# Optimization experiments

Hardware: AMD Instinct MI355X
Metric: run time of the kernel (lower is better)

Reference implementation:

```python
import jax, jax.numpy as jnp
import numpy as np

N_NODES = 100000
N_EDGES = 6400000
F_IN, F_HID, F_OUT = 5, 5, 10


def setup_inputs() -> dict:
    key = jax.random.key(0)
    ks = jax.random.split(key, 9)
    x = jax.random.normal(ks[0], (N_NODES, F_IN), dtype=jnp.float32)
    src = jax.random.randint(ks[1], (N_EDGES,), 0, N_NODES, dtype=jnp.int32)
    dst = jax.random.randint(ks[2], (N_EDGES,), 0, N_NODES, dtype=jnp.int32)
    s1 = 1.0 / np.sqrt(F_IN)
    s2 = 1.0 / np.sqrt(F_HID)
    W_self1 = jax.random.uniform(ks[3], (F_IN, F_HID), jnp.float32, -s1, s1)
    W_neigh1 = jax.random.uniform(ks[4], (F_IN, F_HID), jnp.float32, -s1, s1)
    b1 = jnp.zeros((F_HID,), jnp.float32)
    W_self2 = jax.random.uniform(ks[5], (F_HID, F_OUT), jnp.float32, -s2, s2)
    W_neigh2 = jax.random.uniform(ks[6], (F_HID, F_OUT), jnp.float32, -s2, s2)
    b2 = jnp.zeros((F_OUT,), jnp.float32)
    return {"x": x, "src": src, "dst": dst,
            "W_self1": W_self1, "W_neigh1": W_neigh1, "b1": b1,
            "W_self2": W_self2, "W_neigh2": W_neigh2, "b2": b2}


def _sage_mean(h, src, dst, W_self, W_neigh, b):
    # DGL SAGEConv (mean): out = h @ W_self + mean_{u->v}(h_u) @ W_neigh + b
    msg = h[src]                                        # [E, F] gather
    agg = jax.ops.segment_sum(msg, dst, num_segments=N_NODES)   # [N, F]
    deg = jax.ops.segment_sum(jnp.ones((src.shape[0],), h.dtype), dst,
                              num_segments=N_NODES)     # [N]
    h_neigh = agg / jnp.maximum(deg, 1.0)[:, None]
    return h @ W_self + h_neigh @ W_neigh + b


def reference(x, src, dst, W_self1, W_neigh1, b1, W_self2, W_neigh2, b2):
    h = jax.nn.sigmoid(_sage_mean(x, src, dst, W_self1, W_neigh1, b1))
    out = jax.nn.sigmoid(_sage_mean(h, src, dst, W_self2, W_neigh2, b2))
    return out
```

## Files before the change

kernel.cpp:

```cpp
#include <hip/hip_runtime.h>
#include <math.h>


#define F_IN  5
#define F_HID 5
#define F_OUT 10

#define NBSHIFT 7
#define NPB     (1 << NBSHIFT)
#define MAXNB   1024
#define PBLK    1024
#define CHUNK   8192
#define BSTRIDE 8928
#define SBLK    512
#define LPN2    8
#define LBLK    256

__global__ void init_cursors(int* __restrict__ bcursor, int NB) {
    int t = threadIdx.x;
    if (t < NB) bcursor[t] = t * BSTRIDE;
}

__global__ void partition(const int* __restrict__ src, const int* __restrict__ dst,
                          int* __restrict__ bcursor, int* __restrict__ packed,
                          int E, int NB) {
    __shared__ int h[MAXNB], s[MAXNB], excl[MAXNB], adj[MAXNB];
    __shared__ int buf[CHUNK];
    __shared__ unsigned char dlow[CHUNK];
    int t = threadIdx.x;
    h[t] = 0;
    __syncthreads();
    int base = blockIdx.x * CHUNK;
    int end  = min(base + CHUNK, E);
    for (int i = base + t; i < end; i += PBLK)
        atomicAdd(&h[dst[i] >> NBSHIFT], 1);
    __syncthreads();
    s[t] = h[t];
    __syncthreads();
    for (int off = 1; off < PBLK; off <<= 1) {
        int v = (t >= off) ? s[t - off] : 0;
        __syncthreads();
        s[t] += v;
        __syncthreads();
    }
    excl[t] = s[t] - h[t];
    __syncthreads();
    if (t < NB) {
        int cb = h[t];
        int go = cb ? atomicAdd(&bcursor[t], cb) : 0;
        adj[t] = go - excl[t];
    }
    __syncthreads();
    for (int i = base + t; i < end; i += PBLK) {
        int d = dst[i];
        int b = d >> NBSHIFT;
        int p = atomicAdd(&excl[b], 1);
        buf[p]  = src[i] | (b << 17);
        dlow[p] = (unsigned char)(d & (NPB - 1));
    }
    __syncthreads();
    int cnt = end - base;
    for (int p = t; p < cnt; p += PBLK) {
        int e = buf[p];
        int b = e >> 17;
        packed[adj[b] + p] = (e & 0x1FFFF) | ((int)dlow[p] << 17);
    }
}

__device__ __forceinline__ float sigmoidf(float v) {
    return 1.0f / (1.0f + __expf(-v));
}

__global__ void sortagg1(const float* __restrict__ x, int* __restrict__ packed,
                         const int* __restrict__ bcursor,
                         const float* __restrict__ Ws, const float* __restrict__ Wn,
                         const float* __restrict__ bias,
                         float* __restrict__ hp, int* __restrict__ starts,
                         int* __restrict__ degs, int N) {
    __shared__ int buf[BSTRIDE];
    __shared__ int nhist[NPB], ncur[NPB], nst[NPB];
    int b = blockIdx.x, t = threadIdx.x;
    int s0  = b * BSTRIDE;
    int cnt = min(bcursor[b] - s0, BSTRIDE);
    if (t < NPB) nhist[t] = 0;
    __syncthreads();
    for (int i = t; i < cnt; i += SBLK)
        atomicAdd(&nhist[(packed[s0 + i] >> 17) & (NPB - 1)], 1);
    __syncthreads();
    int v = (t < NPB) ? nhist[t] : 0;
    if (t < NPB) ncur[t] = v;
    __syncthreads();
    for (int off = 1; off < NPB; off <<= 1) {
        int u = (t < NPB && t >= off) ? ncur[t - off] : 0;
        __syncthreads();
        if (t < NPB) ncur[t] += u;
        __syncthreads();
    }
    if (t < NPB) {
        int ex = ncur[t] - v;
        nst[t]  = ex;
        ncur[t] = ex;
        int node = (b << NBSHIFT) + t;
        if (node < N) { starts[node] = s0 + ex; degs[node] = v; }
    }
    __syncthreads();
    for (int i = t; i < cnt; i += SBLK) {
        int e = packed[s0 + i];
        int p = atomicAdd(&ncur[(e >> 17) & (NPB - 1)], 1);
        buf[p] = e;
    }
    __syncthreads();
    for (int i = t; i < cnt; i += SBLK)
        packed[s0 + i] = buf[i] & 0x1FFFF;
    int sub = t & 3, ln = t >> 2;
    int node = (b << NBSHIFT) + ln;
    float a0 = 0, a1 = 0, a2 = 0, a3 = 0, a4 = 0;
    int dg = 0;
    if (node < N) {
        int st = nst[ln];
        dg = nhist[ln];
        for (int k = sub; k < dg; k += 4) {
            int u = buf[st + k] & 0x1FFFF;
            const float* fr = x + (size_t)u * 5;
            float4 a = *(const float4*)fr;
            float  e4 = fr[4];
            a0 += a.x; a1 += a.y; a2 += a.z; a3 += a.w; a4 += e4;
        }
    }
    #pragma unroll
    for (int off = 2; off > 0; off >>= 1) {
        a0 += __shfl_down(a0, off, 4);
        a1 += __shfl_down(a1, off, 4);
        a2 += __shfl_down(a2, off, 4);
        a3 += __shfl_down(a3, off, 4);
        a4 += __shfl_down(a4, off, 4);
    }
    if (sub != 0 || node >= N) return;
    float rd = 1.0f / fmaxf((float)dg, 1.0f);
    float ni[F_IN] = { a0 * rd, a1 * rd, a2 * rd, a3 * rd, a4 * rd };
    float xi[F_IN];
    const float* xr = x + (size_t)node * 5;
    #pragma unroll
    for (int f = 0; f < F_IN; ++f) xi[f] = xr[f];
    #pragma unroll
    for (int j = 0; j < F_HID; ++j) {
        float acc = bias[j];
        #pragma unroll
        for (int f = 0; f < F_IN; ++f)
            acc += xi[f] * Ws[f * F_HID + j] + ni[f] * Wn[f * F_HID + j];
        hp[(size_t)node * 8 + j] = sigmoidf(acc);
    }
}

__global__ void layer2(const float* __restrict__ hp, const int* __restrict__ eidx,
                       const int* __restrict__ starts, const int* __restrict__ degs,
                       const float* __restrict__ Ws, const float* __restrict__ Wn,
                       const float* __restrict__ b,
                       float* __restrict__ out, int N) {
    int tid = blockIdx.x * blockDim.x + threadIdx.x;
    int v   = tid >> 3;
    int sub = threadIdx.x & (LPN2 - 1);
    if (v >= N) return;
    int st = starts[v], dg = degs[v];
    float s0 = 0, s1 = 0, s2 = 0, s3 = 0, s4 = 0;
    for (int k = sub; k < dg; k += LPN2) {
        int u = eidx[st + k];
        const float4 a = *(const float4*)(hp + (size_t)u * 8);
        float a4 = hp[(size_t)u * 8 + 4];
        s0 += a.x; s1 += a.y; s2 += a.z; s3 += a.w; s4 += a4;
    }
    #pragma unroll
    for (int off = LPN2 / 2; off > 0; off >>= 1) {
        s0 += __shfl_down(s0, off, LPN2);
        s1 += __shfl_down(s1, off, LPN2);
        s2 += __shfl_down(s2, off, LPN2);
        s3 += __shfl_down(s3, off, LPN2);
        s4 += __shfl_down(s4, off, LPN2);
    }
    if (sub != 0) return;
    float rd = 1.0f / fmaxf((float)dg, 1.0f);
    float ni[F_HID] = { s0 * rd, s1 * rd, s2 * rd, s3 * rd, s4 * rd };
    float hi[F_HID];
    #pragma unroll
    for (int f = 0; f < F_HID; ++f) hi[f] = hp[(size_t)v * 8 + f];
    #pragma unroll
    for (int j = 0; j < F_OUT; ++j) {
        float acc = b[j];
        #pragma unroll
        for (int f = 0; f < F_HID; ++f)
            acc += hi[f] * Ws[f * F_OUT + j] + ni[f] * Wn[f * F_OUT + j];
        out[(size_t)v * F_OUT + j] = sigmoidf(acc);
    }
}

extern "C" void kernel_launch(void* const* d_in, const int* in_sizes, int n_in,
                              void* d_out, int out_size, void* d_ws, size_t ws_size,
                              hipStream_t stream) {
    const float* x   = (const float*)d_in[0];
    const int*   src = (const int*)d_in[1];
    const int*   dst = (const int*)d_in[2];
    const float* Ws1 = (const float*)d_in[3];
    const float* Wn1 = (const float*)d_in[4];
    const float* b1  = (const float*)d_in[5];
    const float* Ws2 = (const float*)d_in[6];
    const float* Wn2 = (const float*)d_in[7];
    const float* b2  = (const float*)d_in[8];
    float* out = (float*)d_out;

    const int N  = in_sizes[0] / F_IN;
    const int E  = in_sizes[1];
    const int NB = (N + NPB - 1) >> NBSHIFT;

    int*   bcursor = (int*)d_ws;
    int*   starts  = bcursor + 1024;
    int*   degs    = starts + N;
    int*   packed  = degs + N;
    float* hp      = (float*)(packed + (size_t)NB * BSTRIDE);

    const int ablocks = (E + CHUNK - 1) / CHUNK;
    const int lgrid   = ((size_t)N * LPN2 + LBLK - 1) / LBLK;

    init_cursors<<<1, 1024, 0, stream>>>(bcursor, NB);
    partition<<<ablocks, PBLK, 0, stream>>>(src, dst, bcursor, packed, E, NB);
    sortagg1<<<NB, SBLK, 0, stream>>>(x, packed, bcursor, Ws1, Wn1, b1,
                                      hp, starts, degs, N);
    layer2<<<lgrid, LBLK, 0, stream>>>(hp, packed, starts, degs, Ws2, Wn2, b2, out, N);
}
```

Measured before the change: 242.3 us.

## Halve bucket size, cache packed edges in registers, compact hidden features

```diff
diff --git a/kernel.cpp b/kernel.cpp
--- a/kernel.cpp
+++ b/kernel.cpp
@@ -6,49 +6,55 @@
 #define F_HID 5
 #define F_OUT 10
 
-#define NBSHIFT 7
+#define NBSHIFT 6
 #define NPB     (1 << NBSHIFT)
-#define MAXNB   1024
+#define MAXNB   1664
 #define PBLK    1024
-#define CHUNK   8192
-#define BSTRIDE 8928
+#define CHUNK   4096
+#define BSTRIDE 4608
 #define SBLK    512
+#define SPT     9
 #define LPN2    8
-#define LBLK    256
+#define LBLK    512
 
 __global__ void init_cursors(int* __restrict__ bcursor, int NB) {
-    int t = threadIdx.x;
+    int t = blockIdx.x * blockDim.x + threadIdx.x;
     if (t < NB) bcursor[t] = t * BSTRIDE;
 }
 
 __global__ void partition(const int* __restrict__ src, const int* __restrict__ dst,
                           int* __restrict__ bcursor, int* __restrict__ packed,
                           int E, int NB) {
-    __shared__ int h[MAXNB], s[MAXNB], excl[MAXNB], adj[MAXNB];
+    __shared__ int h[MAXNB], excl[MAXNB], adj[MAXNB];
+    __shared__ int scanTmp[PBLK];
     __shared__ int buf[CHUNK];
     __shared__ unsigned char dlow[CHUNK];
     int t = threadIdx.x;
-    h[t] = 0;
+    for (int i = t; i < MAXNB; i += PBLK) h[i] = 0;
     __syncthreads();
     int base = blockIdx.x * CHUNK;
     int end  = min(base + CHUNK, E);
     for (int i = base + t; i < end; i += PBLK)
         atomicAdd(&h[dst[i] >> NBSHIFT], 1);
     __syncthreads();
-    s[t] = h[t];
+    int a0 = h[2 * t];
+    int a1 = h[2 * t + 1];
+    scanTmp[t] = a0 + a1;
     __syncthreads();
     for (int off = 1; off < PBLK; off <<= 1) {
-        int v = (t >= off) ? s[t - off] : 0;
-        __syncthreads();
-        s[t] += v;
-        __syncthreads();
-    }
-    excl[t] = s[t] - h[t];
-    __syncthreads();
-    if (t < NB) {
-        int cb = h[t];
-        int go = cb ? atomicAdd(&bcursor[t], cb) : 0;
-        adj[t] = go - excl[t];
+        int v = (t >= off) ? scanTmp[t - off] : 0;
+        __syncthreads();
+        scanTmp[t] += v;
+        __syncthreads();
+    }
+    int pairExcl = (t == 0) ? 0 : scanTmp[t - 1];
+    excl[2 * t]     = pairExcl;
+    excl[2 * t + 1] = pairExcl + a0;
+    __syncthreads();
+    for (int i = t; i < NB; i += PBLK) {
+        int cb = h[i];
+        int go = cb ? atomicAdd(&bcursor[i], cb) : 0;
+        adj[i] = go - excl[i];
     }
     __syncthreads();
     for (int i = base + t; i < end; i += PBLK) {
@@ -84,8 +90,16 @@
     int cnt = min(bcursor[b] - s0, BSTRIDE);
     if (t < NPB) nhist[t] = 0;
     __syncthreads();
-    for (int i = t; i < cnt; i += SBLK)
-        atomicAdd(&nhist[(packed[s0 + i] >> 17) & (NPB - 1)], 1);
+    int myv[SPT];
+    #pragma unroll
+    for (int j = 0; j < SPT; ++j) {
+        int i = t + j * SBLK;
+        if (i < cnt) {
+            int e = packed[s0 + i];
+            myv[j] = e;
+            atomicAdd(&nhist[(e >> 17) & (NPB - 1)], 1);
+        }
+    }
     __syncthreads();
     int v = (t < NPB) ? nhist[t] : 0;
     if (t < NPB) ncur[t] = v;
@@ -104,22 +118,26 @@
         if (node < N) { starts[node] = s0 + ex; degs[node] = v; }
     }
     __syncthreads();
-    for (int i = t; i < cnt; i += SBLK) {
-        int e = packed[s0 + i];
-        int p = atomicAdd(&ncur[(e >> 17) & (NPB - 1)], 1);
-        buf[p] = e;
+    #pragma unroll
+    for (int j = 0; j < SPT; ++j) {
+        int i = t + j * SBLK;
+        if (i < cnt) {
+            int e = myv[j];
+            int p = atomicAdd(&ncur[(e >> 17) & (NPB - 1)], 1);
+            buf[p] = e;
+        }
     }
     __syncthreads();
     for (int i = t; i < cnt; i += SBLK)
         packed[s0 + i] = buf[i] & 0x1FFFF;
-    int sub = t & 3, ln = t >> 2;
+    int sub = t & 7, ln = t >> 3;
     int node = (b << NBSHIFT) + ln;
     float a0 = 0, a1 = 0, a2 = 0, a3 = 0, a4 = 0;
     int dg = 0;
     if (node < N) {
         int st = nst[ln];
         dg = nhist[ln];
-        for (int k = sub; k < dg; k += 4) {
+        for (int k = sub; k < dg; k += 8) {
             int u = buf[st + k] & 0x1FFFF;
             const float* fr = x + (size_t)u * 5;
             float4 a = *(const float4*)fr;
@@ -128,12 +146,12 @@
         }
     }
     #pragma unroll
-    for (int off = 2; off > 0; off >>= 1) {
-        a0 += __shfl_down(a0, off, 4);
-        a1 += __shfl_down(a1, off, 4);
-        a2 += __shfl_down(a2, off, 4);
-        a3 += __shfl_down(a3, off, 4);
-        a4 += __shfl_down(a4, off, 4);
+    for (int off = 4; off > 0; off >>= 1) {
+        a0 += __shfl_down(a0, off, 8);
+        a1 += __shfl_down(a1, off, 8);
+        a2 += __shfl_down(a2, off, 8);
+        a3 += __shfl_down(a3, off, 8);
+        a4 += __shfl_down(a4, off, 8);
     }
     if (sub != 0 || node >= N) return;
     float rd = 1.0f / fmaxf((float)dg, 1.0f);
@@ -148,7 +166,7 @@
         #pragma unroll
         for (int f = 0; f < F_IN; ++f)
             acc += xi[f] * Ws[f * F_HID + j] + ni[f] * Wn[f * F_HID + j];
-        hp[(size_t)node * 8 + j] = sigmoidf(acc);
+        hp[(size_t)node * 5 + j] = sigmoidf(acc);
     }
 }
 
@@ -165,8 +183,9 @@
     float s0 = 0, s1 = 0, s2 = 0, s3 = 0, s4 = 0;
     for (int k = sub; k < dg; k += LPN2) {
         int u = eidx[st + k];
-        const float4 a = *(const float4*)(hp + (size_t)u * 8);
-        float a4 = hp[(size_t)u * 8 + 4];
+        const float* fr = hp + (size_t)u * 5;
+        float4 a = *(const float4*)fr;
+        float a4 = fr[4];
         s0 += a.x; s1 += a.y; s2 += a.z; s3 += a.w; s4 += a4;
     }
     #pragma unroll
@@ -181,8 +200,9 @@
     float rd = 1.0f / fmaxf((float)dg, 1.0f);
     float ni[F_HID] = { s0 * rd, s1 * rd, s2 * rd, s3 * rd, s4 * rd };
     float hi[F_HID];
-    #pragma unroll
-    for (int f = 0; f < F_HID; ++f) hi[f] = hp[(size_t)v * 8 + f];
+    const float* hr = hp + (size_t)v * 5;
+    #pragma unroll
+    for (int f = 0; f < F_HID; ++f) hi[f] = hr[f];
     #pragma unroll
     for (int j = 0; j < F_OUT; ++j) {
         float acc = b[j];
@@ -212,7 +232,7 @@
     const int NB = (N + NPB - 1) >> NBSHIFT;
 
     int*   bcursor = (int*)d_ws;
-    int*   starts  = bcursor + 1024;
+    int*   starts  = bcursor + 2048;
     int*   degs    = starts + N;
     int*   packed  = degs + N;
     float* hp      = (float*)(packed + (size_t)NB * BSTRIDE);
@@ -220,7 +240,7 @@
     const int ablocks = (E + CHUNK - 1) / CHUNK;
     const int lgrid   = ((size_t)N * LPN2 + LBLK - 1) / LBLK;
 
-    init_cursors<<<1, 1024, 0, stream>>>(bcursor, NB);
+    init_cursors<<<2, 1024, 0, stream>>>(bcursor, NB);
     partition<<<ablocks, PBLK, 0, stream>>>(src, dst, bcursor, packed, E, NB);
     sortagg1<<<NB, SBLK, 0, stream>>>(x, packed, bcursor, Ws1, Wn1, b1,
                                       hp, starts, degs, N);
```

New measurement: 250.3 us. 1.03x slower.

## Cache bucket edges in registers during node sort and compact hidden features

Applied to the files above, without the earlier changes.

```diff
diff --git a/kernel.cpp b/kernel.cpp
--- a/kernel.cpp
+++ b/kernel.cpp
@@ -8,23 +8,23 @@
 
 #define NBSHIFT 7
 #define NPB     (1 << NBSHIFT)
-#define MAXNB   1024
 #define PBLK    1024
 #define CHUNK   8192
-#define BSTRIDE 8928
+#define BSTRIDE 9216
 #define SBLK    512
+#define SPT     18
 #define LPN2    8
 #define LBLK    256
 
 __global__ void init_cursors(int* __restrict__ bcursor, int NB) {
-    int t = threadIdx.x;
+    int t = blockIdx.x * blockDim.x + threadIdx.x;
     if (t < NB) bcursor[t] = t * BSTRIDE;
 }
 
 __global__ void partition(const int* __restrict__ src, const int* __restrict__ dst,
                           int* __restrict__ bcursor, int* __restrict__ packed,
                           int E, int NB) {
-    __shared__ int h[MAXNB], s[MAXNB], excl[MAXNB], adj[MAXNB];
+    __shared__ int h[PBLK], s[PBLK], excl[PBLK], adj[PBLK];
     __shared__ int buf[CHUNK];
     __shared__ unsigned char dlow[CHUNK];
     int t = threadIdx.x;
@@ -84,8 +84,16 @@
     int cnt = min(bcursor[b] - s0, BSTRIDE);
     if (t < NPB) nhist[t] = 0;
     __syncthreads();
-    for (int i = t; i < cnt; i += SBLK)
-        atomicAdd(&nhist[(packed[s0 + i] >> 17) & (NPB - 1)], 1);
+    int myv[SPT];
+    #pragma unroll
+    for (int j = 0; j < SPT; ++j) {
+        int i = t + j * SBLK;
+        if (i < cnt) {
+            int e = packed[s0 + i];
+            myv[j] = e;
+            atomicAdd(&nhist[(e >> 17) & (NPB - 1)], 1);
+        }
+    }
     __syncthreads();
     int v = (t < NPB) ? nhist[t] : 0;
     if (t < NPB) ncur[t] = v;
@@ -104,10 +112,14 @@
         if (node < N) { starts[node] = s0 + ex; degs[node] = v; }
     }
     __syncthreads();
-    for (int i = t; i < cnt; i += SBLK) {
-        int e = packed[s0 + i];
-        int p = atomicAdd(&ncur[(e >> 17) & (NPB - 1)], 1);
-        buf[p] = e;
+    #pragma unroll
+    for (int j = 0; j < SPT; ++j) {
+        int i = t + j * SBLK;
+        if (i < cnt) {
+            int e = myv[j];
+            int p = atomicAdd(&ncur[(e >> 17) & (NPB - 1)], 1);
+            buf[p] = e;
+        }
     }
     __syncthreads();
     for (int i = t; i < cnt; i += SBLK)
@@ -148,7 +160,7 @@
         #pragma unroll
         for (int f = 0; f < F_IN; ++f)
             acc += xi[f] * Ws[f * F_HID + j] + ni[f] * Wn[f * F_HID + j];
-        hp[(size_t)node * 8 + j] = sigmoidf(acc);
+        hp[(size_t)node * 5 + j] = sigmoidf(acc);
     }
 }
 
@@ -165,8 +177,9 @@
     float s0 = 0, s1 = 0, s2 = 0, s3 = 0, s4 = 0;
     for (int k = sub; k < dg; k += LPN2) {
         int u = eidx[st + k];
-        const float4 a = *(const float4*)(hp + (size_t)u * 8);
-        float a4 = hp[(size_t)u * 8 + 4];
+        const float* fr = hp + (size_t)u * 5;
+        float4 a = *(const float4*)fr;
+        float a4 = fr[4];
         s0 += a.x; s1 += a.y; s2 += a.z; s3 += a.w; s4 += a4;
     }
     #pragma unroll
@@ -181,8 +194,9 @@
     float rd = 1.0f / fmaxf((float)dg, 1.0f);
     float ni[F_HID] = { s0 * rd, s1 * rd, s2 * rd, s3 * rd, s4 * rd };
     float hi[F_HID];
-    #pragma unroll
-    for (int f = 0; f < F_HID; ++f) hi[f] = hp[(size_t)v * 8 + f];
+    const float* hr = hp + (size_t)v * 5;
+    #pragma unroll
+    for (int f = 0; f < F_HID; ++f) hi[f] = hr[f];
     #pragma unroll
     for (int j = 0; j < F_OUT; ++j) {
         float acc = b[j];
```

New measurement: 232.5 us. 1.04x faster.
